# Optimization experiments

Hardware: AMD Instinct MI355X
Metric: run time of the kernel (lower is better)

Reference implementation:

```python
import jax, jax.numpy as jnp
import numpy as np

EMBED = 1024
HEADS = 16
HEAD_DIM = EMBED // HEADS


def setup_inputs() -> dict:
    key = jax.random.key(0)
    ks = jax.random.split(key, 5)
    scale = 1.0 / np.sqrt(EMBED)
    x = jax.random.normal(ks[0], (2, 2048, EMBED), dtype=jnp.float32)
    W_qkv = jax.random.normal(ks[1], (EMBED, 3 * EMBED), dtype=jnp.float32) * scale
    b_qkv = jnp.zeros((3 * EMBED,), dtype=jnp.float32)
    W_out = jax.random.normal(ks[2], (EMBED, EMBED), dtype=jnp.float32) * scale
    b_out = jnp.zeros((EMBED,), dtype=jnp.float32)
    return {"x": x, "W_qkv": W_qkv, "b_qkv": b_qkv, "W_out": W_out, "b_out": b_out}


def reference(x, W_qkv, b_qkv, W_out, b_out):
    B, S, E = x.shape
    # fused QKV projection
    qkv = x @ W_qkv + b_qkv                       # [B, S, 3E]
    qkv = qkv.reshape(B, S, HEADS, 3 * HEAD_DIM)
    q, k, v = jnp.split(qkv, 3, axis=-1)          # each [B, S, H, D]
    scale = jnp.sqrt(jnp.asarray(HEAD_DIM, dtype=x.dtype))
    # scores [B, H, S, S]
    scores = jnp.einsum('bqhd,bkhd->bhqk', q, k) / scale
    attn = jax.nn.softmax(scores, axis=-1)
    out = jnp.einsum('bhqk,bkhd->bqhd', attn, v).reshape(B, S, E)
    return out @ W_out + b_out
```

## Files before the change

kernel.cpp:

```cpp
#include <hip/hip_runtime.h>

#define B_    2
#define S_    2048
#define E_    1024
#define H_    16
#define D_    64
#define M_    4096
#define NQKV  3072
#define K_    1024

typedef __bf16 bf16;
typedef __attribute__((ext_vector_type(4))) __bf16 bf16x4;
typedef __attribute__((ext_vector_type(8))) __bf16 bf16x8;
typedef __attribute__((ext_vector_type(4))) float  f32x4;
typedef __attribute__((ext_vector_type(16))) float f32x16;

#define QSCALE 0.18033688f

__device__ __forceinline__ void gload_lds16(const void* g, void* l) {
    __builtin_amdgcn_global_load_lds(
        (const __attribute__((address_space(1))) void*)g,
        (__attribute__((address_space(3))) void*)l, 16, 0, 0);
}

__global__ __launch_bounds__(256) void cast_f32_bf16(
    const float* __restrict__ in, bf16* __restrict__ out, int n)
{
    int i = (blockIdx.x * 256 + threadIdx.x) * 4;
    if (i >= n) return;
    float4 v = *reinterpret_cast<const float4*>(in + i);
    bf16x4 o = { (bf16)v.x, (bf16)v.y, (bf16)v.z, (bf16)v.w };
    *reinterpret_cast<bf16x4*>(out + i) = o;
}

__global__ __launch_bounds__(256) void transpose_cast(
    const float* __restrict__ W, bf16* __restrict__ WT, int Krows, int Ncols)
{
    __shared__ bf16 tile[32][33];
    int bj = blockIdx.x;
    int bi = blockIdx.y;
    int tx = threadIdx.x & 31;
    int ty = threadIdx.x >> 5;
#pragma unroll
    for (int it = 0; it < 4; ++it) {
        int r = ty + it * 8;
        tile[r][tx] = (bf16)W[(size_t)(bi * 32 + r) * Ncols + bj * 32 + tx];
    }
    __syncthreads();
#pragma unroll
    for (int it = 0; it < 4; ++it) {
        int r = ty + it * 8;
        WT[(size_t)(bj * 32 + r) * Krows + bi * 32 + tx] = tile[tx][r];
    }
}

__device__ __forceinline__ void gemm_tile_128(
    const bf16* __restrict__ A, const bf16* __restrict__ BT, int K,
    int bm0, int bn0, f32x4 acc[4][4])
{
    __shared__ bf16 sA[128 * 32];
    __shared__ bf16 sB[128 * 32];
    const int tid  = threadIdx.x;
    const int lane = tid & 63;
    const int wave = tid >> 6;
    const int g    = lane >> 4;
    const int r    = lane & 15;
    const int wr   = wave >> 1, wc = wave & 1;
    const int lrow = lane >> 2;
    const int lcol = (lane & 3) * 8;

#pragma unroll
    for (int m = 0; m < 4; ++m)
#pragma unroll
        for (int n = 0; n < 4; ++n) acc[m][n] = (f32x4){0.f, 0.f, 0.f, 0.f};

    for (int k0 = 0; k0 < K; k0 += 32) {
#pragma unroll
        for (int j = 0; j < 2; ++j) {
            int r0 = wave * 32 + j * 16;
            gload_lds16(A  + (size_t)(bm0 + r0 + lrow) * K + k0 + lcol, &sA[r0 * 32]);
            gload_lds16(BT + (size_t)(bn0 + r0 + lrow) * K + k0 + lcol, &sB[r0 * 32]);
        }
        __syncthreads();
        bf16x8 af[4], bfr[4];
#pragma unroll
        for (int m = 0; m < 4; ++m)
            af[m] = *reinterpret_cast<const bf16x8*>(&sA[(wr * 64 + m * 16 + r) * 32 + g * 8]);
#pragma unroll
        for (int n = 0; n < 4; ++n)
            bfr[n] = *reinterpret_cast<const bf16x8*>(&sB[(wc * 64 + n * 16 + r) * 32 + g * 8]);
        __builtin_amdgcn_s_setprio(1);
#pragma unroll
        for (int m = 0; m < 4; ++m)
#pragma unroll
            for (int n = 0; n < 4; ++n)
                acc[m][n] = __builtin_amdgcn_mfma_f32_16x16x32_bf16(af[m], bfr[n], acc[m][n], 0, 0, 0);
        __builtin_amdgcn_s_setprio(0);
        __syncthreads();
    }
}

__global__ __launch_bounds__(256) void gemm_qkv(
    const bf16* __restrict__ xb, const bf16* __restrict__ WT,
    const float* __restrict__ bias,
    bf16* __restrict__ Qb, bf16* __restrict__ Kb, bf16* __restrict__ Vt)
{
    f32x4 acc[4][4];
    int bm0 = blockIdx.y * 128, bn0 = blockIdx.x * 128;
    gemm_tile_128(xb, WT, K_, bm0, bn0, acc);

    const int lane = threadIdx.x & 63, wave = threadIdx.x >> 6;
    const int g = lane >> 4, c = lane & 15;
    const int wr = wave >> 1, wc = wave & 1;
#pragma unroll
    for (int m = 0; m < 4; ++m) {
        int ibase = bm0 + wr * 64 + m * 16 + 4 * g;
        int b = ibase >> 11, s = ibase & 2047;
#pragma unroll
        for (int n = 0; n < 4; ++n) {
            int j = bn0 + wc * 64 + n * 16 + c;
            int h = j / 192, w = j % 192;
            int t = w >> 6, d = w & 63;
            float bj = bias[j];
            if (t == 2) {
                bf16x4 v4 = { (bf16)(acc[m][n][0] + bj), (bf16)(acc[m][n][1] + bj),
                              (bf16)(acc[m][n][2] + bj), (bf16)(acc[m][n][3] + bj) };
                *reinterpret_cast<bf16x4*>(
                    &Vt[((size_t)((b * H_ + h) * D_ + d)) * S_ + s]) = v4;
            } else {
                bf16* dst = (t == 0) ? Qb : Kb;
                float scale = (t == 0) ? QSCALE : 1.0f;
#pragma unroll
                for (int jj = 0; jj < 4; ++jj) {
                    size_t idx = ((size_t)((b * H_ + h) * S_ + s + jj)) * D_ + d;
                    dst[idx] = (bf16)((acc[m][n][jj] + bj) * scale);
                }
            }
        }
    }
}

__global__ __launch_bounds__(512, 4) void attn_kernel(
    const bf16* __restrict__ Qb, const bf16* __restrict__ Kb,
    const bf16* __restrict__ Vt, bf16* __restrict__ Ob)
{
    __shared__ __align__(16) char smem[37888];

    const int bh  = blockIdx.y;
    const int q0  = blockIdx.x * 128;
    const int tid = threadIdx.x, lane = tid & 63;
    const int qw   = (tid >> 6) & 3;
    const int half = tid >> 8;
    const int gtid = tid & 255;
    const int c = lane & 31;
    const int h = lane >> 5;

    bf16* sKh = reinterpret_cast<bf16*>(smem) + half * (64 * 72);
    bf16* sVh = reinterpret_cast<bf16*>(smem + 18432) + half * (64 * 72);
    float* mrg = reinterpret_cast<float*>(smem);
    float* ml  = reinterpret_cast<float*>(smem + 36864);

    const bf16* Qp = Qb + (size_t)bh * S_ * D_;
    const bf16* Kp = Kb + (size_t)bh * S_ * D_ + (size_t)half * 1024 * D_;
    const bf16* Vp = Vt + (size_t)bh * D_ * S_ + half * 1024;

    const int qrow = q0 + qw * 32 + c;
    bf16x8 qf[4];
#pragma unroll
    for (int kk = 0; kk < 4; ++kk)
        qf[kk] = *reinterpret_cast<const bf16x8*>(Qp + (size_t)qrow * D_ + kk * 16 + 8 * h);

    f32x16 acc[2];
#pragma unroll
    for (int t = 0; t < 2; ++t) acc[t] = (f32x16)(0.f);
    float m_run = -1e30f, l_run = 0.f;

    const int srow = gtid >> 3, sgi = gtid & 7;

    for (int kv0 = 0; kv0 < 1024; kv0 += 64) {
        __syncthreads();
#pragma unroll
        for (int i = 0; i < 2; ++i) {
            int row = srow + i * 32;
            *reinterpret_cast<uint4*>(&sKh[row * 72 + sgi * 8]) =
                *reinterpret_cast<const uint4*>(Kp + (size_t)(kv0 + row) * D_ + sgi * 8);
            *reinterpret_cast<uint4*>(&sVh[row * 72 + sgi * 8]) =
                *reinterpret_cast<const uint4*>(Vp + (size_t)row * S_ + kv0 + sgi * 8);
        }
        __syncthreads();

        f32x16 sc0 = (f32x16)(0.f), sc1 = (f32x16)(0.f);
        __builtin_amdgcn_s_setprio(1);
#pragma unroll
        for (int kk = 0; kk < 4; ++kk) {
            bf16x8 kf0 = *reinterpret_cast<const bf16x8*>(
                &sKh[(c) * 72 + kk * 16 + 8 * h]);
            bf16x8 kf1 = *reinterpret_cast<const bf16x8*>(
                &sKh[(32 + c) * 72 + kk * 16 + 8 * h]);
            sc0 = __builtin_amdgcn_mfma_f32_32x32x16_bf16(kf0, qf[kk], sc0, 0, 0, 0);
            sc1 = __builtin_amdgcn_mfma_f32_32x32x16_bf16(kf1, qf[kk], sc1, 0, 0, 0);
        }
        __builtin_amdgcn_s_setprio(0);

        float a0 = fmaxf(fmaxf(sc0[0], sc0[1]), sc0[2]);
        float a1 = fmaxf(fmaxf(sc0[3], sc0[4]), sc0[5]);
        float a2 = fmaxf(fmaxf(sc0[6], sc0[7]), sc0[8]);
        float a3 = fmaxf(fmaxf(sc0[9], sc0[10]), sc0[11]);
        float a4 = fmaxf(fmaxf(sc0[12], sc0[13]), sc0[14]);
        float a5 = fmaxf(fmaxf(sc1[0], sc1[1]), sc1[2]);
        float a6 = fmaxf(fmaxf(sc1[3], sc1[4]), sc1[5]);
        float a7 = fmaxf(fmaxf(sc1[6], sc1[7]), sc1[8]);
        float a8 = fmaxf(fmaxf(sc1[9], sc1[10]), sc1[11]);
        float a9 = fmaxf(fmaxf(sc1[12], sc1[13]), sc1[14]);
        float b0 = fmaxf(fmaxf(a0, a1), sc0[15]);
        float b1 = fmaxf(fmaxf(a2, a3), a4);
        float b2 = fmaxf(fmaxf(a5, a6), sc1[15]);
        float b3 = fmaxf(fmaxf(a7, a8), a9);
        float vmax = fmaxf(fmaxf(b0, b1), fmaxf(b2, b3));
        vmax = fmaxf(vmax, __shfl_xor(vmax, 32));
        if (__any(vmax > m_run + 8.0f)) {
            float mnew = fmaxf(m_run, vmax);
            float f = exp2f(m_run - mnew);
            l_run *= f;
#pragma unroll
            for (int t = 0; t < 2; ++t) acc[t] *= f;
            m_run = mnew;
        }
        float p0[16], p1[16];
#pragma unroll
        for (int r = 0; r < 16; ++r) p0[r] = exp2f(sc0[r] - m_run);
#pragma unroll
        for (int r = 0; r < 16; ++r) p1[r] = exp2f(sc1[r] - m_run);
        {
            float s0 = ((p0[0] + p0[1]) + (p0[2] + p0[3])) +
                       ((p0[4] + p0[5]) + (p0[6] + p0[7]));
            float s1 = ((p0[8] + p0[9]) + (p0[10] + p0[11])) +
                       ((p0[12] + p0[13]) + (p0[14] + p0[15]));
            float s2 = ((p1[0] + p1[1]) + (p1[2] + p1[3])) +
                       ((p1[4] + p1[5]) + (p1[6] + p1[7]));
            float s3 = ((p1[8] + p1[9]) + (p1[10] + p1[11])) +
                       ((p1[12] + p1[13]) + (p1[14] + p1[15]));
            l_run += (s0 + s1) + (s2 + s3);
        }

        unsigned w0[8], w1[8];
#pragma unroll
        for (int b = 0; b < 4; ++b) {
            union { bf16 x; unsigned short u; } c0, c1, c2, c3, d0, d1, d2, d3;
            c0.x = (bf16)p0[4 * b + 0]; c1.x = (bf16)p0[4 * b + 1];
            c2.x = (bf16)p0[4 * b + 2]; c3.x = (bf16)p0[4 * b + 3];
            d0.x = (bf16)p1[4 * b + 0]; d1.x = (bf16)p1[4 * b + 1];
            d2.x = (bf16)p1[4 * b + 2]; d3.x = (bf16)p1[4 * b + 3];
            w0[2 * b]     = (unsigned)c0.u | ((unsigned)c1.u << 16);
            w0[2 * b + 1] = (unsigned)c2.u | ((unsigned)c3.u << 16);
            w1[2 * b]     = (unsigned)d0.u | ((unsigned)d1.u << 16);
            w1[2 * b + 1] = (unsigned)d2.u | ((unsigned)d3.u << 16);
        }

#pragma unroll
        for (int ks = 0; ks < 2; ++ks) {
            const unsigned* w = ks ? w1 : w0;
#pragma unroll
            for (int kk = 0; kk < 2; ++kk) {
                unsigned s_lo = h ? w[4 * kk]     : w[4 * kk + 2];
                unsigned s_hi = h ? w[4 * kk + 1] : w[4 * kk + 3];
                unsigned r_lo = __shfl_xor(s_lo, 32);
                unsigned r_hi = __shfl_xor(s_hi, 32);
                union { bf16x8 v; unsigned u[4]; } pf;
                if (h == 0) {
                    pf.u[0] = w[4 * kk]; pf.u[1] = w[4 * kk + 1];
                    pf.u[2] = r_lo;      pf.u[3] = r_hi;
                } else {
                    pf.u[0] = r_lo;      pf.u[1] = r_hi;
                    pf.u[2] = w[4 * kk + 2]; pf.u[3] = w[4 * kk + 3];
                }
                __builtin_amdgcn_s_setprio(1);
#pragma unroll
                for (int t = 0; t < 2; ++t) {
                    bf16x8 vf = *reinterpret_cast<const bf16x8*>(
                        &sVh[(32 * t + c) * 72 + ks * 32 + kk * 16 + 8 * h]);
                    acc[t] = __builtin_amdgcn_mfma_f32_32x32x16_bf16(vf, pf.v, acc[t], 0, 0, 0);
                }
                __builtin_amdgcn_s_setprio(0);
            }
        }
    }

    float l_tot = l_run + __shfl_xor(l_run, 32);

    __syncthreads();
    if (half == 1) {
        float4* dst = reinterpret_cast<float4*>(&mrg[(qw * 64 + lane) * 33]);
#pragma unroll
        for (int t = 0; t < 2; ++t)
#pragma unroll
            for (int v = 0; v < 4; ++v)
                dst[t * 4 + v] = make_float4(acc[t][4 * v + 0], acc[t][4 * v + 1],
                                             acc[t][4 * v + 2], acc[t][4 * v + 3]);
        if (lane < 32) { ml[(qw * 32 + lane) * 2 + 0] = m_run;
                         ml[(qw * 32 + lane) * 2 + 1] = l_tot; }
    }
    __syncthreads();

    if (half == 0) {
        float m1 = ml[(qw * 32 + c) * 2 + 0], l1 = ml[(qw * 32 + c) * 2 + 1];
        float mm = fmaxf(m_run, m1);
        float f0 = exp2f(m_run - mm), f1 = exp2f(m1 - mm);
        float li = 1.0f / (l_tot * f0 + l1 * f1);
        float g0 = f0 * li, g1 = f1 * li;
        const float4* src = reinterpret_cast<const float4*>(&mrg[(qw * 64 + lane) * 33]);
        float o[2][16];
#pragma unroll
        for (int t = 0; t < 2; ++t)
#pragma unroll
            for (int v = 0; v < 4; ++v) {
                float4 a1 = src[t * 4 + v];
                o[t][4 * v + 0] = acc[t][4 * v + 0] * g0 + a1.x * g1;
                o[t][4 * v + 1] = acc[t][4 * v + 1] * g0 + a1.y * g1;
                o[t][4 * v + 2] = acc[t][4 * v + 2] * g0 + a1.z * g1;
                o[t][4 * v + 3] = acc[t][4 * v + 3] * g0 + a1.w * g1;
            }

        bf16* so = reinterpret_cast<bf16*>(&mrg[(size_t)qw * 64 * 33]);
#pragma unroll
        for (int t = 0; t < 2; ++t)
#pragma unroll
            for (int b = 0; b < 4; ++b) {
                bf16x4 v4 = { (bf16)o[t][4 * b + 0], (bf16)o[t][4 * b + 1],
                              (bf16)o[t][4 * b + 2], (bf16)o[t][4 * b + 3] };
                *reinterpret_cast<bf16x4*>(&so[c * 72 + t * 32 + b * 8 + 4 * h]) = v4;
            }
        const int bb = bh >> 4, hh = bh & 15;
#pragma unroll
        for (int i = 0; i < 4; ++i) {
            int chunk = lane + 64 * i;
            int row = chunk >> 3, gi = chunk & 7;
            uint4 val = *reinterpret_cast<uint4*>(&so[row * 72 + gi * 8]);
            *reinterpret_cast<uint4*>(
                Ob + ((size_t)(bb * S_ + q0 + qw * 32 + row)) * E_ + hh * 64 + gi * 8) = val;
        }
    }
}

__global__ __launch_bounds__(256) void gemm_out(
    const bf16* __restrict__ Ob, const bf16* __restrict__ WT,
    const float* __restrict__ bias, float* __restrict__ out)
{
    f32x4 acc[4][4];
    int bm0 = blockIdx.y * 128, bn0 = blockIdx.x * 128;
    gemm_tile_128(Ob, WT, K_, bm0, bn0, acc);

    const int lane = threadIdx.x & 63, wave = threadIdx.x >> 6;
    const int g = lane >> 4, c = lane & 15;
    const int wr = wave >> 1, wc = wave & 1;
#pragma unroll
    for (int m = 0; m < 4; ++m) {
        int ibase = bm0 + wr * 64 + m * 16 + 4 * g;
#pragma unroll
        for (int n = 0; n < 4; ++n) {
            int j = bn0 + wc * 64 + n * 16 + c;
            float bj = bias[j];
#pragma unroll
            for (int jj = 0; jj < 4; ++jj) {
                int row = ibase + jj;
                out[(size_t)row * E_ + j] = acc[m][n][jj] + bj;
            }
        }
    }
}

extern "C" void kernel_launch(void* const* d_in, const int* in_sizes, int n_in,
                              void* d_out, int out_size, void* d_ws, size_t ws_size,
                              hipStream_t stream)
{
    const float* x     = (const float*)d_in[0];
    const float* W_qkv = (const float*)d_in[1];
    const float* b_qkv = (const float*)d_in[2];
    const float* W_out = (const float*)d_in[3];
    const float* b_out = (const float*)d_in[4];
    float* out = (float*)d_out;

    char* ws = (char*)d_ws;
    bf16* xb    = (bf16*)(ws);
    bf16* WqkvT = (bf16*)(ws + (8u  << 20));
    bf16* WoutT = (bf16*)(ws + (14u << 20));
    bf16* Qb    = (bf16*)(ws + (16u << 20));
    bf16* Kb    = (bf16*)(ws + (24u << 20));
    bf16* Vt    = (bf16*)(ws + (32u << 20));
    bf16* Ob    = (bf16*)(ws + (40u << 20));

    cast_f32_bf16<<<4096, 256, 0, stream>>>(x, xb, M_ * K_);
    transpose_cast<<<dim3(NQKV / 32, K_ / 32), 256, 0, stream>>>(W_qkv, WqkvT, K_, NQKV);
    transpose_cast<<<dim3(E_ / 32, K_ / 32), 256, 0, stream>>>(W_out, WoutT, K_, E_);
    gemm_qkv<<<dim3(NQKV / 128, M_ / 128), 256, 0, stream>>>(xb, WqkvT, b_qkv, Qb, Kb, Vt);
    attn_kernel<<<dim3(S_ / 128, B_ * H_), 512, 0, stream>>>(Qb, Kb, Vt, Ob);
    gemm_out<<<dim3(E_ / 128, M_ / 128), 256, 0, stream>>>(Ob, WoutT, b_out, out);
}
```

Measured before the change: 146.0 us.

## Merge prep kernels into one launch and double attention KV tile per sync

The three preprocessing launches (x cast and two weight transpose-casts) are merged into a single block-indexed prep kernel, removing two launch gaps. The attention kernel now stages 128 keys and values per iteration instead of 64 and processes them in two unrolled 64-key phases. This halves the number of barrier pairs and lengthens each global load batch. In exchange, shared memory grows from about 37 KB to 72 KB per block, which may lower occupancy below the declared four blocks per CU.

```diff
diff --git a/kernel.cpp b/kernel.cpp
--- a/kernel.cpp
+++ b/kernel.cpp
@@ -23,22 +23,30 @@
         (__attribute__((address_space(3))) void*)l, 16, 0, 0);
 }
 
-__global__ __launch_bounds__(256) void cast_f32_bf16(
-    const float* __restrict__ in, bf16* __restrict__ out, int n)
-{
-    int i = (blockIdx.x * 256 + threadIdx.x) * 4;
-    if (i >= n) return;
-    float4 v = *reinterpret_cast<const float4*>(in + i);
-    bf16x4 o = { (bf16)v.x, (bf16)v.y, (bf16)v.z, (bf16)v.w };
-    *reinterpret_cast<bf16x4*>(out + i) = o;
-}
-
-__global__ __launch_bounds__(256) void transpose_cast(
-    const float* __restrict__ W, bf16* __restrict__ WT, int Krows, int Ncols)
+__global__ __launch_bounds__(256) void prep_kernel(
+    const float* __restrict__ x,     bf16* __restrict__ xb,
+    const float* __restrict__ W_qkv, bf16* __restrict__ WqkvT,
+    const float* __restrict__ W_out, bf16* __restrict__ WoutT)
 {
     __shared__ bf16 tile[32][33];
-    int bj = blockIdx.x;
-    int bi = blockIdx.y;
+    const int bid = blockIdx.x;
+    if (bid < 4096) {
+        int i = (bid * 256 + threadIdx.x) * 4;
+        float4 v = *reinterpret_cast<const float4*>(x + i);
+        bf16x4 o = { (bf16)v.x, (bf16)v.y, (bf16)v.z, (bf16)v.w };
+        *reinterpret_cast<bf16x4*>(xb + i) = o;
+        return;
+    }
+    const float* W; bf16* WT; int Ncols, bj, bi;
+    if (bid < 4096 + 3072) {
+        int t = bid - 4096;
+        W = W_qkv; WT = WqkvT; Ncols = NQKV;
+        bj = t % 96; bi = t / 96;
+    } else {
+        int t = bid - 7168;
+        W = W_out; WT = WoutT; Ncols = E_;
+        bj = t % 32; bi = t / 32;
+    }
     int tx = threadIdx.x & 31;
     int ty = threadIdx.x >> 5;
 #pragma unroll
@@ -50,7 +58,7 @@
 #pragma unroll
     for (int it = 0; it < 4; ++it) {
         int r = ty + it * 8;
-        WT[(size_t)(bj * 32 + r) * Krows + bi * 32 + tx] = tile[tx][r];
+        WT[(size_t)(bj * 32 + r) * K_ + bi * 32 + tx] = tile[tx][r];
     }
 }
 
@@ -144,7 +152,7 @@
     const bf16* __restrict__ Qb, const bf16* __restrict__ Kb,
     const bf16* __restrict__ Vt, bf16* __restrict__ Ob)
 {
-    __shared__ __align__(16) char smem[37888];
+    __shared__ __align__(16) char smem[72704];
 
     const int bh  = blockIdx.y;
     const int q0  = blockIdx.x * 128;
@@ -155,10 +163,10 @@
     const int c = lane & 31;
     const int h = lane >> 5;
 
-    bf16* sKh = reinterpret_cast<bf16*>(smem) + half * (64 * 72);
-    bf16* sVh = reinterpret_cast<bf16*>(smem + 18432) + half * (64 * 72);
+    bf16* sKh = reinterpret_cast<bf16*>(smem) + half * (128 * 72);
+    bf16* sVh = reinterpret_cast<bf16*>(smem + 36864) + half * (64 * 136);
     float* mrg = reinterpret_cast<float*>(smem);
-    float* ml  = reinterpret_cast<float*>(smem + 36864);
+    float* ml  = reinterpret_cast<float*>(smem + 71680);
 
     const bf16* Qp = Qb + (size_t)bh * S_ * D_;
     const bf16* Kp = Kb + (size_t)bh * S_ * D_ + (size_t)half * 1024 * D_;
@@ -175,113 +183,119 @@
     for (int t = 0; t < 2; ++t) acc[t] = (f32x16)(0.f);
     float m_run = -1e30f, l_run = 0.f;
 
-    const int srow = gtid >> 3, sgi = gtid & 7;
-
-    for (int kv0 = 0; kv0 < 1024; kv0 += 64) {
+    const int srowK = gtid >> 3, sgiK = (gtid & 7) * 8;
+    const int srowV = gtid >> 4, sgiV = (gtid & 15) * 8;
+
+    for (int kv0 = 0; kv0 < 1024; kv0 += 128) {
         __syncthreads();
 #pragma unroll
-        for (int i = 0; i < 2; ++i) {
-            int row = srow + i * 32;
-            *reinterpret_cast<uint4*>(&sKh[row * 72 + sgi * 8]) =
-                *reinterpret_cast<const uint4*>(Kp + (size_t)(kv0 + row) * D_ + sgi * 8);
-            *reinterpret_cast<uint4*>(&sVh[row * 72 + sgi * 8]) =
-                *reinterpret_cast<const uint4*>(Vp + (size_t)row * S_ + kv0 + sgi * 8);
+        for (int i = 0; i < 4; ++i) {
+            int rK = srowK + i * 32;
+            *reinterpret_cast<uint4*>(&sKh[rK * 72 + sgiK]) =
+                *reinterpret_cast<const uint4*>(Kp + (size_t)(kv0 + rK) * D_ + sgiK);
+            int rV = srowV + i * 16;
+            *reinterpret_cast<uint4*>(&sVh[rV * 136 + sgiV]) =
+                *reinterpret_cast<const uint4*>(Vp + (size_t)rV * S_ + kv0 + sgiV);
         }
         __syncthreads();
 
-        f32x16 sc0 = (f32x16)(0.f), sc1 = (f32x16)(0.f);
-        __builtin_amdgcn_s_setprio(1);
-#pragma unroll
-        for (int kk = 0; kk < 4; ++kk) {
-            bf16x8 kf0 = *reinterpret_cast<const bf16x8*>(
-                &sKh[(c) * 72 + kk * 16 + 8 * h]);
-            bf16x8 kf1 = *reinterpret_cast<const bf16x8*>(
-                &sKh[(32 + c) * 72 + kk * 16 + 8 * h]);
-            sc0 = __builtin_amdgcn_mfma_f32_32x32x16_bf16(kf0, qf[kk], sc0, 0, 0, 0);
-            sc1 = __builtin_amdgcn_mfma_f32_32x32x16_bf16(kf1, qf[kk], sc1, 0, 0, 0);
-        }
-        __builtin_amdgcn_s_setprio(0);
-
-        float a0 = fmaxf(fmaxf(sc0[0], sc0[1]), sc0[2]);
-        float a1 = fmaxf(fmaxf(sc0[3], sc0[4]), sc0[5]);
-        float a2 = fmaxf(fmaxf(sc0[6], sc0[7]), sc0[8]);
-        float a3 = fmaxf(fmaxf(sc0[9], sc0[10]), sc0[11]);
-        float a4 = fmaxf(fmaxf(sc0[12], sc0[13]), sc0[14]);
-        float a5 = fmaxf(fmaxf(sc1[0], sc1[1]), sc1[2]);
-        float a6 = fmaxf(fmaxf(sc1[3], sc1[4]), sc1[5]);
-        float a7 = fmaxf(fmaxf(sc1[6], sc1[7]), sc1[8]);
-        float a8 = fmaxf(fmaxf(sc1[9], sc1[10]), sc1[11]);
-        float a9 = fmaxf(fmaxf(sc1[12], sc1[13]), sc1[14]);
-        float b0 = fmaxf(fmaxf(a0, a1), sc0[15]);
-        float b1 = fmaxf(fmaxf(a2, a3), a4);
-        float b2 = fmaxf(fmaxf(a5, a6), sc1[15]);
-        float b3 = fmaxf(fmaxf(a7, a8), a9);
-        float vmax = fmaxf(fmaxf(b0, b1), fmaxf(b2, b3));
-        vmax = fmaxf(vmax, __shfl_xor(vmax, 32));
-        if (__any(vmax > m_run + 8.0f)) {
-            float mnew = fmaxf(m_run, vmax);
-            float f = exp2f(m_run - mnew);
-            l_run *= f;
-#pragma unroll
-            for (int t = 0; t < 2; ++t) acc[t] *= f;
-            m_run = mnew;
-        }
-        float p0[16], p1[16];
-#pragma unroll
-        for (int r = 0; r < 16; ++r) p0[r] = exp2f(sc0[r] - m_run);
-#pragma unroll
-        for (int r = 0; r < 16; ++r) p1[r] = exp2f(sc1[r] - m_run);
-        {
-            float s0 = ((p0[0] + p0[1]) + (p0[2] + p0[3])) +
-                       ((p0[4] + p0[5]) + (p0[6] + p0[7]));
-            float s1 = ((p0[8] + p0[9]) + (p0[10] + p0[11])) +
-                       ((p0[12] + p0[13]) + (p0[14] + p0[15]));
-            float s2 = ((p1[0] + p1[1]) + (p1[2] + p1[3])) +
-                       ((p1[4] + p1[5]) + (p1[6] + p1[7]));
-            float s3 = ((p1[8] + p1[9]) + (p1[10] + p1[11])) +
-                       ((p1[12] + p1[13]) + (p1[14] + p1[15]));
-            l_run += (s0 + s1) + (s2 + s3);
-        }
-
-        unsigned w0[8], w1[8];
-#pragma unroll
-        for (int b = 0; b < 4; ++b) {
-            union { bf16 x; unsigned short u; } c0, c1, c2, c3, d0, d1, d2, d3;
-            c0.x = (bf16)p0[4 * b + 0]; c1.x = (bf16)p0[4 * b + 1];
-            c2.x = (bf16)p0[4 * b + 2]; c3.x = (bf16)p0[4 * b + 3];
-            d0.x = (bf16)p1[4 * b + 0]; d1.x = (bf16)p1[4 * b + 1];
-            d2.x = (bf16)p1[4 * b + 2]; d3.x = (bf16)p1[4 * b + 3];
-            w0[2 * b]     = (unsigned)c0.u | ((unsigned)c1.u << 16);
-            w0[2 * b + 1] = (unsigned)c2.u | ((unsigned)c3.u << 16);
-            w1[2 * b]     = (unsigned)d0.u | ((unsigned)d1.u << 16);
-            w1[2 * b + 1] = (unsigned)d2.u | ((unsigned)d3.u << 16);
-        }
-
-#pragma unroll
-        for (int ks = 0; ks < 2; ++ks) {
-            const unsigned* w = ks ? w1 : w0;
-#pragma unroll
-            for (int kk = 0; kk < 2; ++kk) {
-                unsigned s_lo = h ? w[4 * kk]     : w[4 * kk + 2];
-                unsigned s_hi = h ? w[4 * kk + 1] : w[4 * kk + 3];
-                unsigned r_lo = __shfl_xor(s_lo, 32);
-                unsigned r_hi = __shfl_xor(s_hi, 32);
-                union { bf16x8 v; unsigned u[4]; } pf;
-                if (h == 0) {
-                    pf.u[0] = w[4 * kk]; pf.u[1] = w[4 * kk + 1];
-                    pf.u[2] = r_lo;      pf.u[3] = r_hi;
-                } else {
-                    pf.u[0] = r_lo;      pf.u[1] = r_hi;
-                    pf.u[2] = w[4 * kk + 2]; pf.u[3] = w[4 * kk + 3];
+#pragma unroll
+        for (int ph = 0; ph < 2; ++ph) {
+            const int base = ph * 64;
+            f32x16 sc0 = (f32x16)(0.f), sc1 = (f32x16)(0.f);
+            __builtin_amdgcn_s_setprio(1);
+#pragma unroll
+            for (int kk = 0; kk < 4; ++kk) {
+                bf16x8 kf0 = *reinterpret_cast<const bf16x8*>(
+                    &sKh[(base + c) * 72 + kk * 16 + 8 * h]);
+                bf16x8 kf1 = *reinterpret_cast<const bf16x8*>(
+                    &sKh[(base + 32 + c) * 72 + kk * 16 + 8 * h]);
+                sc0 = __builtin_amdgcn_mfma_f32_32x32x16_bf16(kf0, qf[kk], sc0, 0, 0, 0);
+                sc1 = __builtin_amdgcn_mfma_f32_32x32x16_bf16(kf1, qf[kk], sc1, 0, 0, 0);
+            }
+            __builtin_amdgcn_s_setprio(0);
+
+            float a0 = fmaxf(fmaxf(sc0[0], sc0[1]), sc0[2]);
+            float a1 = fmaxf(fmaxf(sc0[3], sc0[4]), sc0[5]);
+            float a2 = fmaxf(fmaxf(sc0[6], sc0[7]), sc0[8]);
+            float a3 = fmaxf(fmaxf(sc0[9], sc0[10]), sc0[11]);
+            float a4 = fmaxf(fmaxf(sc0[12], sc0[13]), sc0[14]);
+            float a5 = fmaxf(fmaxf(sc1[0], sc1[1]), sc1[2]);
+            float a6 = fmaxf(fmaxf(sc1[3], sc1[4]), sc1[5]);
+            float a7 = fmaxf(fmaxf(sc1[6], sc1[7]), sc1[8]);
+            float a8 = fmaxf(fmaxf(sc1[9], sc1[10]), sc1[11]);
+            float a9 = fmaxf(fmaxf(sc1[12], sc1[13]), sc1[14]);
+            float b0 = fmaxf(fmaxf(a0, a1), sc0[15]);
+            float b1 = fmaxf(fmaxf(a2, a3), a4);
+            float b2 = fmaxf(fmaxf(a5, a6), sc1[15]);
+            float b3 = fmaxf(fmaxf(a7, a8), a9);
+            float vmax = fmaxf(fmaxf(b0, b1), fmaxf(b2, b3));
+            vmax = fmaxf(vmax, __shfl_xor(vmax, 32));
+            if (__any(vmax > m_run + 8.0f)) {
+                float mnew = fmaxf(m_run, vmax);
+                float f = exp2f(m_run - mnew);
+                l_run *= f;
+#pragma unroll
+                for (int t = 0; t < 2; ++t) acc[t] *= f;
+                m_run = mnew;
+            }
+            float p0[16], p1[16];
+#pragma unroll
+            for (int r = 0; r < 16; ++r) p0[r] = exp2f(sc0[r] - m_run);
+#pragma unroll
+            for (int r = 0; r < 16; ++r) p1[r] = exp2f(sc1[r] - m_run);
+            {
+                float s0 = ((p0[0] + p0[1]) + (p0[2] + p0[3])) +
+                           ((p0[4] + p0[5]) + (p0[6] + p0[7]));
+                float s1 = ((p0[8] + p0[9]) + (p0[10] + p0[11])) +
+                           ((p0[12] + p0[13]) + (p0[14] + p0[15]));
+                float s2 = ((p1[0] + p1[1]) + (p1[2] + p1[3])) +
+                           ((p1[4] + p1[5]) + (p1[6] + p1[7]));
+                float s3 = ((p1[8] + p1[9]) + (p1[10] + p1[11])) +
+                           ((p1[12] + p1[13]) + (p1[14] + p1[15]));
+                l_run += (s0 + s1) + (s2 + s3);
+            }
+
+            unsigned w0[8], w1[8];
+#pragma unroll
+            for (int b = 0; b < 4; ++b) {
+                union { bf16 x; unsigned short u; } c0, c1, c2, c3, d0, d1, d2, d3;
+                c0.x = (bf16)p0[4 * b + 0]; c1.x = (bf16)p0[4 * b + 1];
+                c2.x = (bf16)p0[4 * b + 2]; c3.x = (bf16)p0[4 * b + 3];
+                d0.x = (bf16)p1[4 * b + 0]; d1.x = (bf16)p1[4 * b + 1];
+                d2.x = (bf16)p1[4 * b + 2]; d3.x = (bf16)p1[4 * b + 3];
+                w0[2 * b]     = (unsigned)c0.u | ((unsigned)c1.u << 16);
+                w0[2 * b + 1] = (unsigned)c2.u | ((unsigned)c3.u << 16);
+                w1[2 * b]     = (unsigned)d0.u | ((unsigned)d1.u << 16);
+                w1[2 * b + 1] = (unsigned)d2.u | ((unsigned)d3.u << 16);
+            }
+
+#pragma unroll
+            for (int ks = 0; ks < 2; ++ks) {
+                const unsigned* w = ks ? w1 : w0;
+#pragma unroll
+                for (int kk = 0; kk < 2; ++kk) {
+                    unsigned s_lo = h ? w[4 * kk]     : w[4 * kk + 2];
+                    unsigned s_hi = h ? w[4 * kk + 1] : w[4 * kk + 3];
+                    unsigned r_lo = __shfl_xor(s_lo, 32);
+                    unsigned r_hi = __shfl_xor(s_hi, 32);
+                    union { bf16x8 v; unsigned u[4]; } pf;
+                    if (h == 0) {
+                        pf.u[0] = w[4 * kk]; pf.u[1] = w[4 * kk + 1];
+                        pf.u[2] = r_lo;      pf.u[3] = r_hi;
+                    } else {
+                        pf.u[0] = r_lo;      pf.u[1] = r_hi;
+                        pf.u[2] = w[4 * kk + 2]; pf.u[3] = w[4 * kk + 3];
+                    }
+                    __builtin_amdgcn_s_setprio(1);
+#pragma unroll
+                    for (int t = 0; t < 2; ++t) {
+                        bf16x8 vf = *reinterpret_cast<const bf16x8*>(
+                            &sVh[(32 * t + c) * 136 + base + ks * 32 + kk * 16 + 8 * h]);
+                        acc[t] = __builtin_amdgcn_mfma_f32_32x32x16_bf16(vf, pf.v, acc[t], 0, 0, 0);
+                    }
+                    __builtin_amdgcn_s_setprio(0);
                 }
-                __builtin_amdgcn_s_setprio(1);
-#pragma unroll
-                for (int t = 0; t < 2; ++t) {
-                    bf16x8 vf = *reinterpret_cast<const bf16x8*>(
-                        &sVh[(32 * t + c) * 72 + ks * 32 + kk * 16 + 8 * h]);
-                    acc[t] = __builtin_amdgcn_mfma_f32_32x32x16_bf16(vf, pf.v, acc[t], 0, 0, 0);
-                }
-                __builtin_amdgcn_s_setprio(0);
             }
         }
     }
@@ -389,9 +403,7 @@
     bf16* Vt    = (bf16*)(ws + (32u << 20));
     bf16* Ob    = (bf16*)(ws + (40u << 20));
 
-    cast_f32_bf16<<<4096, 256, 0, stream>>>(x, xb, M_ * K_);
-    transpose_cast<<<dim3(NQKV / 32, K_ / 32), 256, 0, stream>>>(W_qkv, WqkvT, K_, NQKV);
-    transpose_cast<<<dim3(E_ / 32, K_ / 32), 256, 0, stream>>>(W_out, WoutT, K_, E_);
+    prep_kernel<<<8192, 256, 0, stream>>>(x, xb, W_qkv, WqkvT, W_out, WoutT);
     gemm_qkv<<<dim3(NQKV / 128, M_ / 128), 256, 0, stream>>>(xb, WqkvT, b_qkv, Qb, Kb, Vt);
     attn_kernel<<<dim3(S_ / 128, B_ * H_), 512, 0, stream>>>(Qb, Kb, Vt, Ob);
     gemm_out<<<dim3(E_ / 128, M_ / 128), 256, 0, stream>>>(Ob, WoutT, b_out, out);
```

Result: faster. 140.8 us (-3.6%).
